# Kernel optimization log

Hardware: AMD Instinct MI355X
Metric: run time of the kernel (lower is better)

Reference implementation:

```python
import jax, jax.numpy as jnp
import numpy as np

N_NODES = 100000
N_EDGES = 3200000
IN_DIM = 128
OUT_DIM = 128


def setup_inputs() -> dict:
    key = jax.random.key(0)
    k1, k2, k3, k4, k5 = jax.random.split(key, 5)
    features = jax.random.normal(k1, (N_NODES, IN_DIM), dtype=jnp.float32)
    edge_src = jax.random.randint(k2, (N_EDGES,), 0, N_NODES, dtype=jnp.int32)
    edge_dst = jax.random.randint(k3, (N_EDGES,), 0, N_NODES, dtype=jnp.int32)
    edge_vals = jax.random.uniform(k4, (N_EDGES,), dtype=jnp.float32)
    # kaiming_normal_ on [in, out] with fan_in = in
    weight = jax.random.normal(k5, (IN_DIM, OUT_DIM), dtype=jnp.float32) * np.sqrt(2.0 / IN_DIM)
    bias = jnp.zeros((OUT_DIM,), dtype=jnp.float32)
    return {
        "features": features,
        "edge_src": edge_src,
        "edge_dst": edge_dst,
        "edge_vals": edge_vals,
        "weight": weight,
        "bias": bias,
    }


def reference(features, edge_src, edge_dst, edge_vals, weight, bias):
    # h = X @ W  : [N, out]
    h = features @ weight
    # SpMM: out[dst] += A[dst, src] * h[src]   (COO edge-list aggregation)
    msgs = h[edge_src] * edge_vals[:, None]          # [E, out]
    agg = jax.ops.segment_sum(msgs, edge_dst, num_segments=N_NODES)
    return agg + bias
```

## Files before the change

kernel.cpp:

```cpp
#include <hip/hip_runtime.h>

#define IN_DIM 128
#define OUT_DIM 128
#define BIN_SHIFT 7
#define BIN_NODES 128
#define NBIN_MAX 800
#define NPART 8
#define CAPX 1024
#define CAP_LDS 4864
#define TILE_A 3072

typedef __attribute__((ext_vector_type(8))) short bf16x8;
typedef __attribute__((ext_vector_type(4))) float f32x4;
typedef __attribute__((ext_vector_type(2))) float f32x2;

__device__ inline unsigned short f2bf(float f) {
    unsigned u = __float_as_uint(f);
    unsigned r = (u + 0x7fff + ((u >> 16) & 1)) >> 16;
    return (unsigned short)r;
}
__device__ inline float bflo(unsigned h) { return __uint_as_float(h << 16); }
__device__ inline float bfhi(unsigned h) { return __uint_as_float(h & 0xffff0000u); }

__global__ __launch_bounds__(256) void pack_w_zero(const float* __restrict__ W,
                                                   unsigned short* __restrict__ Wpack,
                                                   int* __restrict__ gcur, int nbin8) {
    int idx = blockIdx.x * 256 + threadIdx.x;
    if (idx < nbin8) gcur[idx] = 0;
    if (idx >= 16384) return;
    int j = idx & 7;
    int lane = (idx >> 3) & 63;
    int kc = (idx >> 9) & 3;
    int tn = idx >> 11;
    int k = kc * 32 + (lane >> 4) * 8 + j;
    int n = tn * 16 + (lane & 15);
    Wpack[idx] = f2bf(W[k * OUT_DIM + n]);
}

struct BinSmem {
    int2 eL[TILE_A];
    int hist[NBIN_MAX];
    int s0[NBIN_MAX];
    int s1[NBIN_MAX];
    unsigned short bL[TILE_A];
    unsigned short idx[TILE_A];
    unsigned short bS[TILE_A];
};

__global__ __launch_bounds__(256) void phase1(
    const int* __restrict__ src, const int* __restrict__ dst,
    const float* __restrict__ vals, int* __restrict__ gcur,
    int2* __restrict__ entries, int n_edges, int nbin, int nA,
    const float* __restrict__ X, const unsigned short* __restrict__ Wpack,
    unsigned short* __restrict__ Hb, int n_rows, int nG) {
    __shared__ BinSmem sm;

    int b = blockIdx.x;
    int isGemm, widx;
    if (b < 2 * nG) {
        isGemm = (b & 1) == 0;
        widx = b >> 1;
    } else {
        isGemm = 0;
        widx = nG + (b - 2 * nG);
    }

    const int tid = threadIdx.x;

    if (!isGemm) {
        const int part = widx & (NPART - 1);
        const int base = widx * TILE_A;
        const int n0 = n_edges - base;
        if (n0 <= 0) return;
        const int n = (n0 < TILE_A) ? n0 : TILE_A;

        for (int i = tid; i < nbin; i += 256) sm.hist[i] = 0;
        __syncthreads();

        for (int i = tid; i < n; i += 256) {
            int d = dst[base + i];
            int s = src[base + i];
            float v = vals[base + i];
            int bin = d >> BIN_SHIFT;
            sm.eL[i] = make_int2(s | ((d & (BIN_NODES - 1)) << 17), __float_as_int(v));
            sm.bL[i] = (unsigned short)bin;
            atomicAdd(&sm.hist[bin], 1);
        }
        __syncthreads();

        for (int l = tid; l < nbin; l += 256) sm.s0[l] = sm.hist[l];
        __syncthreads();
        int* sin = sm.s0;
        int* sout = sm.s1;
        for (int dd = 1; dd < nbin; dd <<= 1) {
            for (int l = tid; l < nbin; l += 256)
                sout[l] = sin[l] + ((l >= dd) ? sin[l - dd] : 0);
            __syncthreads();
            int* t = sin; sin = sout; sout = t;
        }

        for (int l = tid; l < nbin; l += 256) {
            int c = sm.hist[l];
            int ex = sin[l] - c;
            int g = (c > 0) ? atomicAdd(&gcur[part * nbin + l], c) : 0;
            sout[l] = g - ex;
            sm.hist[l] = ex;
        }
        __syncthreads();

        for (int i = tid; i < n; i += 256) {
            int bb = sm.bL[i];
            int p = atomicAdd(&sm.hist[bb], 1);
            sm.idx[p] = (unsigned short)i;
            sm.bS[p] = (unsigned short)bb;
        }
        __syncthreads();

        for (int p = tid; p < n; p += 256) {
            int bb = sm.bS[p];
            int gp = sout[bb] + p;
            if (gp < CAPX)
                entries[((long long)(part * nbin + bb)) * CAPX + gp] = sm.eL[sm.idx[p]];
        }
        return;
    }

    int strip = widx * 4 + (tid >> 6);
    long long m0 = (long long)strip * 32;
    if (m0 >= n_rows) return;
    int lane = tid & 63;
    int quad = lane >> 4;
    int low = lane & 15;

    const bf16x8* B = (const bf16x8*)Wpack;

    long long r0 = m0 + low;
    long long r1 = m0 + 16 + low;
    if (r1 >= n_rows) r1 = n_rows - 1;
    if (r0 >= n_rows) r0 = n_rows - 1;

    f32x4 acc[2][8] = {};

#pragma unroll
    for (int kc = 0; kc < 4; ++kc) {
        const float4* p0 = (const float4*)(X + r0 * IN_DIM + kc * 32 + quad * 8);
        const float4* p1 = (const float4*)(X + r1 * IN_DIM + kc * 32 + quad * 8);
        float4 x0a = p0[0], x0b = p0[1];
        float4 x1a = p1[0], x1b = p1[1];
        bf16x8 afr0, afr1;
        afr0[0] = f2bf(x0a.x); afr0[1] = f2bf(x0a.y); afr0[2] = f2bf(x0a.z); afr0[3] = f2bf(x0a.w);
        afr0[4] = f2bf(x0b.x); afr0[5] = f2bf(x0b.y); afr0[6] = f2bf(x0b.z); afr0[7] = f2bf(x0b.w);
        afr1[0] = f2bf(x1a.x); afr1[1] = f2bf(x1a.y); afr1[2] = f2bf(x1a.z); afr1[3] = f2bf(x1a.w);
        afr1[4] = f2bf(x1b.x); afr1[5] = f2bf(x1b.y); afr1[6] = f2bf(x1b.z); afr1[7] = f2bf(x1b.w);
#pragma unroll
        for (int tn = 0; tn < 8; ++tn) {
            bf16x8 bfr = B[(tn * 4 + kc) * 64 + lane];
            acc[0][tn] = __builtin_amdgcn_mfma_f32_16x16x32_bf16(afr0, bfr, acc[0][tn], 0, 0, 0);
            acc[1][tn] = __builtin_amdgcn_mfma_f32_16x16x32_bf16(afr1, bfr, acc[1][tn], 0, 0, 0);
        }
    }

#pragma unroll
    for (int t = 0; t < 2; ++t) {
#pragma unroll
        for (int tn = 0; tn < 8; ++tn) {
#pragma unroll
            for (int r = 0; r < 4; ++r) {
                long long row = m0 + t * 16 + quad * 4 + r;
                if (row < n_rows) {
                    int col = tn * 16 + low;
                    Hb[row * OUT_DIM + col] = f2bf(acc[t][tn][r]);
                }
            }
        }
    }
}

__global__ __launch_bounds__(512) void binB_gather(
    const int2* __restrict__ entries, const int* __restrict__ gcur,
    const unsigned short* __restrict__ Hb, const float* __restrict__ bias,
    float* __restrict__ out, int n_nodes, int nbin) {
    __shared__ int2 ent[CAP_LDS];
    __shared__ int hist[BIN_NODES];
    __shared__ int dbase[BIN_NODES];
    __shared__ int cur[BIN_NODES];

    const int bin = blockIdx.x;
    const int tid = threadIdx.x;

    int scnt[NPART], sbase_[NPART];
    int tot = 0;
#pragma unroll
    for (int s = 0; s < NPART; ++s) {
        int c = gcur[s * nbin + bin];
        scnt[s] = (c < CAPX) ? c : CAPX;
        sbase_[s] = tot;
        tot += scnt[s];
    }

    if (tid < BIN_NODES) hist[tid] = 0;
    __syncthreads();

    int2 e[2 * NPART];
    bool ok[2 * NPART];
#pragma unroll
    for (int s = 0; s < NPART; ++s) {
#pragma unroll
        for (int k = 0; k < 2; ++k) {
            int i = tid + k * 512;
            int idx = s * 2 + k;
            ok[idx] = (i < scnt[s]) && (sbase_[s] + i < CAP_LDS);
            if (ok[idx]) e[idx] = entries[((long long)(s * nbin + bin)) * CAPX + i];
        }
    }
#pragma unroll
    for (int idx = 0; idx < 2 * NPART; ++idx)
        if (ok[idx]) atomicAdd(&hist[(e[idx].x >> 17) & (BIN_NODES - 1)], 1);
    __syncthreads();

    if (tid < BIN_NODES) dbase[tid] = hist[tid];
    __syncthreads();
    for (int d = 1; d < BIN_NODES; d <<= 1) {
        int v = 0;
        if (tid < BIN_NODES && tid >= d) v = dbase[tid - d];
        __syncthreads();
        if (tid < BIN_NODES) dbase[tid] += v;
        __syncthreads();
    }
    if (tid < BIN_NODES) {
        int ex = dbase[tid] - hist[tid];
        dbase[tid] = ex;
        cur[tid] = ex;
    }
    __syncthreads();

#pragma unroll
    for (int idx = 0; idx < 2 * NPART; ++idx)
        if (ok[idx]) {
            int l = (e[idx].x >> 17) & (BIN_NODES - 1);
            int pos = atomicAdd(&cur[l], 1);
            ent[pos] = e[idx];
        }
    __syncthreads();

    const int wave = tid >> 6;
    const int lane = tid & 63;
    const int node0 = bin * BIN_NODES;
    float2 bb = ((const float2*)bias)[lane];
    const unsigned short* hrow = Hb + lane * 2;

    for (int ln = wave * 16; ln < wave * 16 + 16; ++ln) {
        int node = node0 + ln;
        if (node >= n_nodes) break;
        int beg = dbase[ln];
        int end = beg + hist[ln];

        f32x2 acc;
        acc[0] = bb.x; acc[1] = bb.y;

        int i = beg;
        for (; i + 16 <= end; i += 16) {
            unsigned h[16];
            float v[16];
#pragma unroll
            for (int j = 0; j < 16; ++j) {
                int2 c = ent[i + j];
                v[j] = __int_as_float(c.y);
                h[j] = *(const unsigned*)(hrow + (long long)(c.x & 0x1ffff) * OUT_DIM);
            }
#pragma unroll
            for (int j = 0; j < 16; ++j) {
                f32x2 hv; hv[0] = bflo(h[j]); hv[1] = bfhi(h[j]);
                f32x2 vv; vv[0] = v[j]; vv[1] = v[j];
                acc += vv * hv;
            }
        }
        for (; i + 8 <= end; i += 8) {
            unsigned h[8];
            float v[8];
#pragma unroll
            for (int j = 0; j < 8; ++j) {
                int2 c = ent[i + j];
                v[j] = __int_as_float(c.y);
                h[j] = *(const unsigned*)(hrow + (long long)(c.x & 0x1ffff) * OUT_DIM);
            }
#pragma unroll
            for (int j = 0; j < 8; ++j) {
                f32x2 hv; hv[0] = bflo(h[j]); hv[1] = bfhi(h[j]);
                f32x2 vv; vv[0] = v[j]; vv[1] = v[j];
                acc += vv * hv;
            }
        }
        for (; i < end; ++i) {
            int2 c0 = ent[i];
            unsigned h0 = *(const unsigned*)(hrow + (long long)(c0.x & 0x1ffff) * OUT_DIM);
            float v = __int_as_float(c0.y);
            f32x2 hv; hv[0] = bflo(h0); hv[1] = bfhi(h0);
            f32x2 vv; vv[0] = v; vv[1] = v;
            acc += vv * hv;
        }

        float2 res; res.x = acc[0]; res.y = acc[1];
        ((float2*)(out + (long long)node * OUT_DIM))[lane] = res;
    }
}

extern "C" void kernel_launch(void* const* d_in, const int* in_sizes, int n_in,
                              void* d_out, int out_size, void* d_ws, size_t ws_size,
                              hipStream_t stream) {
    const float* features  = (const float*)d_in[0];
    const int* edge_src    = (const int*)d_in[1];
    const int* edge_dst    = (const int*)d_in[2];
    const float* edge_vals = (const float*)d_in[3];
    const float* weight    = (const float*)d_in[4];
    const float* bias      = (const float*)d_in[5];

    const int n_nodes = in_sizes[0] / IN_DIM;
    const int n_edges = in_sizes[1];
    const int nbin = (n_nodes + BIN_NODES - 1) / BIN_NODES;

    int2* entries       = (int2*)d_ws;
    unsigned short* Hb  = (unsigned short*)(entries + (long long)NPART * nbin * CAPX);
    unsigned short* Wp  = Hb + (long long)n_nodes * OUT_DIM;
    int* gcur           = (int*)(Wp + 16384);

    float* out = (float*)d_out;

    pack_w_zero<<<64, 256, 0, stream>>>(weight, Wp, gcur, NPART * nbin);

    const int nA = (n_edges + TILE_A - 1) / TILE_A;
    const int n_strips = (n_nodes + 31) / 32;
    const int nG = (n_strips + 3) / 4;
    phase1<<<nA + nG, 256, 0, stream>>>(edge_src, edge_dst, edge_vals, gcur,
                                        entries, n_edges, nbin, nA,
                                        features, Wp, Hb, n_nodes, nG);

    binB_gather<<<nbin, 512, 0, stream>>>(entries, gcur, Hb, bias, out, n_nodes, nbin);
}
```

Measured before the change: 294.1 us.

## Sort gather entries by source range and sweep ranges in lockstep across waves

The gather kernel now sorts each bin's edges by a composite key of destination node and source-node range (8 ranges), and moves to 1024-thread blocks. Each wave keeps 8 node accumulators and processes one source range at a time, with a block barrier between ranges. The aim is to confine concurrent Hb reads from all waves to a narrow slice of the source rows so they hit in L2/MALL cache. The cost is a larger 1024-entry prefix scan, extra barriers, per-iteration bounds predication, and more accumulator registers at 1024 threads per block.

```diff
diff --git a/kernel.cpp b/kernel.cpp
--- a/kernel.cpp
+++ b/kernel.cpp
@@ -9,6 +9,8 @@
 #define CAPX 1024
 #define CAP_LDS 4864
 #define TILE_A 3072
+#define NR 8
+#define NKEY (BIN_NODES * NR)
 
 typedef __attribute__((ext_vector_type(8))) short bf16x8;
 typedef __attribute__((ext_vector_type(4))) float f32x4;
@@ -176,14 +178,14 @@
     }
 }
 
-__global__ __launch_bounds__(512) void binB_gather(
+__global__ __launch_bounds__(1024) void binB_gather(
     const int2* __restrict__ entries, const int* __restrict__ gcur,
     const unsigned short* __restrict__ Hb, const float* __restrict__ bias,
     float* __restrict__ out, int n_nodes, int nbin) {
     __shared__ int2 ent[CAP_LDS];
-    __shared__ int hist[BIN_NODES];
-    __shared__ int dbase[BIN_NODES];
-    __shared__ int cur[BIN_NODES];
+    __shared__ int hist[NKEY];
+    __shared__ int dbase[NKEY];
+    __shared__ int cur[NKEY];
 
     const int bin = blockIdx.x;
     const int tid = threadIdx.x;
@@ -198,110 +200,100 @@
         tot += scnt[s];
     }
 
-    if (tid < BIN_NODES) hist[tid] = 0;
-    __syncthreads();
-
-    int2 e[2 * NPART];
-    bool ok[2 * NPART];
+    hist[tid] = 0;
+    __syncthreads();
+
+    const unsigned rdiv = (unsigned)((n_nodes + NR - 1) / NR);
+    int2 e[NPART];
+    int key[NPART];
+    bool ok[NPART];
 #pragma unroll
     for (int s = 0; s < NPART; ++s) {
-#pragma unroll
-        for (int k = 0; k < 2; ++k) {
-            int i = tid + k * 512;
-            int idx = s * 2 + k;
-            ok[idx] = (i < scnt[s]) && (sbase_[s] + i < CAP_LDS);
-            if (ok[idx]) e[idx] = entries[((long long)(s * nbin + bin)) * CAPX + i];
-        }
-    }
-#pragma unroll
-    for (int idx = 0; idx < 2 * NPART; ++idx)
-        if (ok[idx]) atomicAdd(&hist[(e[idx].x >> 17) & (BIN_NODES - 1)], 1);
-    __syncthreads();
-
-    if (tid < BIN_NODES) dbase[tid] = hist[tid];
-    __syncthreads();
-    for (int d = 1; d < BIN_NODES; d <<= 1) {
-        int v = 0;
-        if (tid < BIN_NODES && tid >= d) v = dbase[tid - d];
-        __syncthreads();
-        if (tid < BIN_NODES) dbase[tid] += v;
-        __syncthreads();
-    }
-    if (tid < BIN_NODES) {
+        ok[s] = (tid < scnt[s]) && (sbase_[s] + tid < CAP_LDS);
+        if (ok[s]) e[s] = entries[((long long)(s * nbin + bin)) * CAPX + tid];
+    }
+#pragma unroll
+    for (int s = 0; s < NPART; ++s)
+        if (ok[s]) {
+            int ld = (e[s].x >> 17) & (BIN_NODES - 1);
+            int rg = (int)((unsigned)(e[s].x & 0x1ffff) / rdiv);
+            key[s] = ld * NR + rg;
+            atomicAdd(&hist[key[s]], 1);
+        }
+    __syncthreads();
+
+    dbase[tid] = hist[tid];
+    __syncthreads();
+    for (int d = 1; d < NKEY; d <<= 1) {
+        int v = (tid >= d) ? dbase[tid - d] : 0;
+        __syncthreads();
+        dbase[tid] += v;
+        __syncthreads();
+    }
+    {
         int ex = dbase[tid] - hist[tid];
+        __syncthreads();
         dbase[tid] = ex;
         cur[tid] = ex;
     }
     __syncthreads();
 
 #pragma unroll
-    for (int idx = 0; idx < 2 * NPART; ++idx)
-        if (ok[idx]) {
-            int l = (e[idx].x >> 17) & (BIN_NODES - 1);
-            int pos = atomicAdd(&cur[l], 1);
-            ent[pos] = e[idx];
+    for (int s = 0; s < NPART; ++s)
+        if (ok[s]) {
+            int pos = atomicAdd(&cur[key[s]], 1);
+            ent[pos] = e[s];
         }
     __syncthreads();
 
     const int wave = tid >> 6;
     const int lane = tid & 63;
-    const int node0 = bin * BIN_NODES;
+    const unsigned short* hrow = Hb + lane * 2;
     float2 bb = ((const float2*)bias)[lane];
-    const unsigned short* hrow = Hb + lane * 2;
-
-    for (int ln = wave * 16; ln < wave * 16 + 16; ++ln) {
-        int node = node0 + ln;
-        if (node >= n_nodes) break;
-        int beg = dbase[ln];
-        int end = beg + hist[ln];
-
-        f32x2 acc;
-        acc[0] = bb.x; acc[1] = bb.y;
-
-        int i = beg;
-        for (; i + 16 <= end; i += 16) {
-            unsigned h[16];
-            float v[16];
-#pragma unroll
-            for (int j = 0; j < 16; ++j) {
-                int2 c = ent[i + j];
-                v[j] = __int_as_float(c.y);
-                h[j] = *(const unsigned*)(hrow + (long long)(c.x & 0x1ffff) * OUT_DIM);
+
+    f32x2 acc[8];
+#pragma unroll
+    for (int k = 0; k < 8; ++k) { acc[k][0] = bb.x; acc[k][1] = bb.y; }
+
+    for (int r = 0; r < NR; ++r) {
+#pragma unroll
+        for (int k = 0; k < 8; ++k) {
+            const int kk = (wave * 8 + k) * NR + r;
+            const int beg = dbase[kk];
+            const int end = beg + hist[kk];
+            for (int i = beg; i < end; i += 8) {
+                unsigned h[8];
+                float v[8];
+                bool okj[8];
+#pragma unroll
+                for (int j = 0; j < 8; ++j) {
+                    okj[j] = (i + j < end);
+                    if (okj[j]) {
+                        int2 c = ent[i + j];
+                        v[j] = __int_as_float(c.y);
+                        h[j] = *(const unsigned*)(hrow + (long long)(c.x & 0x1ffff) * OUT_DIM);
+                    }
+                }
+#pragma unroll
+                for (int j = 0; j < 8; ++j)
+                    if (okj[j]) {
+                        f32x2 hv; hv[0] = bflo(h[j]); hv[1] = bfhi(h[j]);
+                        f32x2 vv; vv[0] = v[j]; vv[1] = v[j];
+                        acc[k] += vv * hv;
+                    }
             }
-#pragma unroll
-            for (int j = 0; j < 16; ++j) {
-                f32x2 hv; hv[0] = bflo(h[j]); hv[1] = bfhi(h[j]);
-                f32x2 vv; vv[0] = v[j]; vv[1] = v[j];
-                acc += vv * hv;
-            }
-        }
-        for (; i + 8 <= end; i += 8) {
-            unsigned h[8];
-            float v[8];
-#pragma unroll
-            for (int j = 0; j < 8; ++j) {
-                int2 c = ent[i + j];
-                v[j] = __int_as_float(c.y);
-                h[j] = *(const unsigned*)(hrow + (long long)(c.x & 0x1ffff) * OUT_DIM);
-            }
-#pragma unroll
-            for (int j = 0; j < 8; ++j) {
-                f32x2 hv; hv[0] = bflo(h[j]); hv[1] = bfhi(h[j]);
-                f32x2 vv; vv[0] = v[j]; vv[1] = v[j];
-                acc += vv * hv;
-            }
-        }
-        for (; i < end; ++i) {
-            int2 c0 = ent[i];
-            unsigned h0 = *(const unsigned*)(hrow + (long long)(c0.x & 0x1ffff) * OUT_DIM);
-            float v = __int_as_float(c0.y);
-            f32x2 hv; hv[0] = bflo(h0); hv[1] = bfhi(h0);
-            f32x2 vv; vv[0] = v; vv[1] = v;
-            acc += vv * hv;
-        }
-
-        float2 res; res.x = acc[0]; res.y = acc[1];
-        ((float2*)(out + (long long)node * OUT_DIM))[lane] = res;
+        }
+        __syncthreads();
+    }
+
+    const int node0 = bin * BIN_NODES + wave * 8;
+#pragma unroll
+    for (int k = 0; k < 8; ++k) {
+        int node = node0 + k;
+        if (node < n_nodes) {
+            float2 res; res.x = acc[k][0]; res.y = acc[k][1];
+            ((float2*)(out + (long long)node * OUT_DIM))[lane] = res;
+        }
     }
 }
 
@@ -335,5 +327,5 @@
                                         entries, n_edges, nbin, nA,
                                         features, Wp, Hb, n_nodes, nG);
 
-    binB_gather<<<nbin, 512, 0, stream>>>(entries, gcur, Hb, bias, out, n_nodes, nbin);
-}
+    binB_gather<<<nbin, 1024, 0, stream>>>(entries, gcur, Hb, bias, out, n_nodes, nbin);
+}
```

Result: slower. 337.4 us (+14.7%).
